# Optimization experiments

Measured on AMD Instinct MI355X. Metric: run time of the kernel, lower is better.

Reference implementation:

```python
import jax, jax.numpy as jnp
import numpy as np

B, G, NPA, NT, L = 8192, 689, 16, 131, 6
S = G + NPA * NT  # 2785 = 689 genes + 16 nodes per each of 131 assemblies


def setup_inputs() -> dict:
    key = jax.random.key(0)
    ks = jax.random.split(key, 8)
    x = jax.random.normal(ks[0], (B, G), dtype=jnp.float32)
    # depth-0 mask: place the 689 gene inputs into the first 689 slots of the layer
    lm0 = jnp.zeros((G, S), jnp.float32).at[jnp.arange(G), jnp.arange(G)].set(1.0)
    # per-depth sparse binary connectivity masks (ontology DAG edges at each depth)
    lm = (jax.random.uniform(ks[1], (L, S, S)) < 0.02).astype(jnp.float32)
    # diagonal pass-through masks for edges skipping this depth (stored as diagonals)
    flm_diag = (jax.random.uniform(ks[2], (L, S)) < 0.3).astype(jnp.float32)
    # final assembly selector: the nodes_per_assembly slots of the root assembly
    fasm = jnp.zeros((S,), jnp.float32).at[G:G + NPA].set(1.0)
    W0 = jax.random.normal(ks[3], (G, S), dtype=jnp.float32) * 0.05
    b0 = jnp.zeros((S,), jnp.float32)
    W = jax.random.normal(ks[4], (L, S, S), dtype=jnp.float32) * 0.05
    b = jnp.zeros((L, S), jnp.float32)
    gamma = jnp.ones((L + 1, S), jnp.float32)
    beta = jnp.zeros((L + 1, S), jnp.float32)
    w_out = jax.random.normal(ks[5], (S,), dtype=jnp.float32) * 0.05
    b_out = jnp.zeros((), jnp.float32)
    return {"x": x, "lm0": lm0, "lm": lm, "flm_diag": flm_diag, "fasm": fasm,
            "W0": W0, "b0": b0, "W": W, "b": b, "gamma": gamma, "beta": beta,
            "w_out": w_out, "b_out": b_out}


def _bn(h, g, bt, eps=1e-5):
    # training-mode BatchNorm1d over the batch axis
    m = h.mean(axis=0)
    v = h.var(axis=0)
    return (h - m) * jax.lax.rsqrt(v + eps) * g + bt


def reference(x, lm0, lm, flm_diag, fasm, W0, b0, W, b, gamma, beta, w_out, b_out):
    # depth 0: masked linear placing genes into layer slots, BN before activation
    h = jnp.tanh(_bn(x @ (W0 * lm0) + b0, gamma[0], beta[0]))  # [B, S]
    def step(h, layer):
        Wl, bl, lml, dl, gl, btl = layer
        # masked linear + BN + activation, plus diagonal pass-through skip
        hn = jnp.tanh(_bn(h @ (Wl * lml) + bl, gl, btl)) + h * dl
        return hn, None
    h, _ = jax.lax.scan(step, h, (W, b, lm, flm_diag, gamma[1:], beta[1:]))
    # output_method='final': linear head on final-assembly nodes only
    return (h * fasm) @ w_out + b_out  # [B]
```

## Files before the change

### kernel.cpp

```cpp
#include <hip/hip_runtime.h>
#include <hip/hip_fp16.h>
#include <stdint.h>

typedef uint32_t u32;
typedef uint64_t u64;
typedef unsigned int v4u __attribute__((ext_vector_type(4)));
typedef float v4f __attribute__((ext_vector_type(4)));
typedef _Float16 v2h __attribute__((ext_vector_type(2)));

constexpr int CB   = 8192;
constexpr int CG   = 689;
constexpr int CL   = 6;
constexpr int CS   = 2785;
constexpr int CSP  = 2816;
constexpr int CRS  = 8256;
constexpr int KCAP = 112;

union V16 { v4u u; v2h h2[4]; };
union F4  { v4f v; float f[4]; u32 u[4]; };
union HW  { u32 u; v2h h; };

__global__ __launch_bounds__(256) void build_main(const float* __restrict__ lm,
                                                  const float* __restrict__ W,
                                                  u64* __restrict__ ent,
                                                  int* __restrict__ cnt)
{
    int rb = blockIdx.x;
    int l  = rb / CS;
    int j  = rb - l * CS;
    const float* lrow = lm + (size_t)rb * CS;
    const float* wrow = W  + (size_t)rb * CS;
    u64 hi = ((u64)((u32)j * (u32)(CRS * 2))) << 32;
    int colbase = l * CSP;

    for (int s4 = threadIdx.x * 4; s4 < CS; s4 += 1024) {
        if (s4 + 4 <= CS) {
            F4 m4; m4.v = *reinterpret_cast<const v4f*>(lrow + s4);
            if ((m4.u[0] | m4.u[1] | m4.u[2] | m4.u[3]) == 0u) continue;
            F4 w4; w4.v = *reinterpret_cast<const v4f*>(wrow + s4);
#pragma unroll
            for (int q = 0; q < 4; q++) {
                if (m4.f[q] != 0.0f) {
                    int s = s4 + q;
                    int pos = atomicAdd(&cnt[colbase + s], 1);
                    if (pos < KCAP) {
                        u32 hw = (u32)__half_as_ushort(__float2half(w4.f[q]));
                        ent[(size_t)(colbase + s) * KCAP + pos] = hi | (u64)(hw | (hw << 16));
                    }
                }
            }
        } else {
            for (int s = s4; s < CS; s++) {
                float m = lrow[s];
                if (m != 0.0f) {
                    int pos = atomicAdd(&cnt[colbase + s], 1);
                    if (pos < KCAP) {
                        u32 hw = (u32)__half_as_ushort(__float2half(wrow[s]));
                        ent[(size_t)(colbase + s) * KCAP + pos] = hi | (u64)(hw | (hw << 16));
                    }
                }
            }
        }
    }
}

__global__ __launch_bounds__(256) void build0(const float* __restrict__ lm0,
                                              const float* __restrict__ W0,
                                              u64* __restrict__ ent,
                                              int* __restrict__ cnt)
{
    int j = blockIdx.x;
    const float* lrow = lm0 + (size_t)j * CS;
    const float* wrow = W0  + (size_t)j * CS;
    u64 hi = ((u64)((u32)j * (u32)(CRS * 2))) << 32;
    for (int s4 = threadIdx.x * 4; s4 < CS; s4 += 1024) {
        if (s4 + 4 <= CS) {
            F4 m4; m4.v = *reinterpret_cast<const v4f*>(lrow + s4);
            if ((m4.u[0] | m4.u[1] | m4.u[2] | m4.u[3]) == 0u) continue;
            F4 w4; w4.v = *reinterpret_cast<const v4f*>(wrow + s4);
#pragma unroll
            for (int q = 0; q < 4; q++) {
                if (m4.f[q] != 0.0f) {
                    int s = s4 + q;
                    int pos = atomicAdd(&cnt[s], 1);
                    if (pos < KCAP) {
                        u32 hw = (u32)__half_as_ushort(__float2half(w4.f[q]));
                        ent[(size_t)s * KCAP + pos] = hi | (u64)(hw | (hw << 16));
                    }
                }
            }
        } else {
            for (int s = s4; s < CS; s++) {
                float m = lrow[s];
                if (m != 0.0f) {
                    int pos = atomicAdd(&cnt[s], 1);
                    if (pos < KCAP) {
                        u32 hw = (u32)__half_as_ushort(__float2half(wrow[s]));
                        ent[(size_t)s * KCAP + pos] = hi | (u64)(hw | (hw << 16));
                    }
                }
            }
        }
    }
}

__global__ __launch_bounds__(256) void transpose_x(const float* __restrict__ x,
                                                   __half* __restrict__ xT)
{
    __shared__ float tile[32][33];
    int gx = blockIdx.x * 32;
    int gy = blockIdx.y * 32;
    int tx = threadIdx.x, ty = threadIdx.y;
#pragma unroll
    for (int i = 0; i < 32; i += 8) {
        int g = gx + tx;
        int b = gy + ty + i;
        tile[ty + i][tx] = (g < CG) ? x[(size_t)b * CG + g] : 0.f;
    }
    __syncthreads();
#pragma unroll
    for (int i = 0; i < 32; i += 8) {
        int g = gx + ty + i;
        int b = gy + tx;
        if (g < CG) xT[(size_t)g * CRS + b] = __float2half(tile[tx][ty + i]);
    }
}

__global__ __launch_bounds__(64) void gather_k(const __half* __restrict__ src,
                                               __half* __restrict__ dst,
                                               const u64* __restrict__ ent,
                                               const int* __restrict__ cnt,
                                               const float* __restrict__ bias,
                                               float* __restrict__ sumv,
                                               float* __restrict__ sumq,
                                               const int* __restrict__ sel,
                                               const int* __restrict__ selcnt)
{
    int s;
    if (sel) {
        if ((int)blockIdx.y >= *selcnt) return;
        s = sel[blockIdx.y];
    } else {
        s = blockIdx.y;
    }
    int lane = threadIdx.x;
    int boff = blockIdx.z * 4096 + blockIdx.x * 512 + lane * 8;

    int n = cnt[s]; if (n > KCAP) n = KCAP;
    int ng = (n + 7) >> 3;
    const u64* e = ent + (size_t)s * KCAP;
    const char* sb = (const char*)src + (size_t)boff * 2;

    float bv = bias[s];
    float acc[8];
#pragma unroll
    for (int j = 0; j < 8; j++) acc[j] = bv;

    for (int g = 0; g < ng; g++) {
        u64 ev[8];
#pragma unroll
        for (int q = 0; q < 8; q++) ev[q] = e[g * 8 + q];
        V16 rv[8];
#pragma unroll
        for (int q = 0; q < 8; q++)
            rv[q].u = *reinterpret_cast<const v4u*>(sb + (u32)(ev[q] >> 32));
#pragma unroll
        for (int q = 0; q < 8; q++) {
            HW w2; w2.u = (u32)ev[q];
#pragma unroll
            for (int j = 0; j < 4; j++) {
                float2 a2;
                a2.x = acc[2*j]; a2.y = acc[2*j+1];
#if __has_builtin(__builtin_amdgcn_fdot2)
#endif
                (void)a2;
                float2 f = __half22float2(*(const __half2*)&rv[q].h2[j]);
                float w = __half2float(*(const __half*)&w2.h);
                acc[2*j]   = fmaf(w, f.x, acc[2*j]);
                acc[2*j+1] = fmaf(w, f.y, acc[2*j+1]);
            }
        }
    }

    V16 o;
#pragma unroll
    for (int j = 0; j < 4; j++) {
        v2h p; p.x = (_Float16)acc[2*j]; p.y = (_Float16)acc[2*j+1];
        o.h2[j] = p;
    }
    __builtin_nontemporal_store(o.u, reinterpret_cast<v4u*>(dst + (size_t)s * CRS + boff));

    float ls = 0.f, lq = 0.f;
#pragma unroll
    for (int j = 0; j < 8; j++) { ls += acc[j]; lq += acc[j] * acc[j]; }
#pragma unroll
    for (int off = 32; off > 0; off >>= 1) {
        ls += __shfl_xor(ls, off);
        lq += __shfl_xor(lq, off);
    }
    if (lane == 0) { atomicAdd(&sumv[s], ls); atomicAdd(&sumq[s], lq); }
}

__global__ __launch_bounds__(64) void bn_act(__half* __restrict__ h,
                                             const __half* __restrict__ prev,
                                             const float* __restrict__ sumv,
                                             const float* __restrict__ sumq,
                                             const float* __restrict__ gamma,
                                             const float* __restrict__ beta,
                                             const float* __restrict__ dlv)
{
    int s = blockIdx.y;
    int boff = blockIdx.x * 512 + threadIdx.x * 8;
    float mean = sumv[s] * (1.0f / CB);
    float var  = sumq[s] * (1.0f / CB) - mean * mean;
    float rstd = rsqrtf(var + 1e-5f);
    float scale = gamma[s] * rstd;
    float shift = beta[s] - mean * scale;
    size_t base = (size_t)s * CRS + boff;
    V16 v; v.u = *reinterpret_cast<const v4u*>(h + base);
    V16 pv;
    float d = 0.f;
    if (prev) { d = dlv[s]; pv.u = *reinterpret_cast<const v4u*>(prev + base); }
    V16 o;
#pragma unroll
    for (int j = 0; j < 4; j++) {
        float2 f = __half22float2(*(const __half2*)&v.h2[j]);
        float t0 = tanhf(fmaf(f.x, scale, shift));
        float t1 = tanhf(fmaf(f.y, scale, shift));
        if (prev) {
            float2 p = __half22float2(*(const __half2*)&pv.h2[j]);
            t0 = fmaf(d, p.x, t0);
            t1 = fmaf(d, p.y, t1);
        }
        v2h pk; pk.x = (_Float16)t0; pk.y = (_Float16)t1;
        o.h2[j] = pk;
    }
    *reinterpret_cast<v4u*>(h + base) = o.u;
}

__global__ __launch_bounds__(256) void head_prep(const float* __restrict__ fasm,
                                                 const float* __restrict__ wout,
                                                 int* __restrict__ hcnt,
                                                 int* __restrict__ hs,
                                                 float* __restrict__ hc)
{
    int s = blockIdx.x * 256 + threadIdx.x;
    if (s >= CS) return;
    float c = fasm[s] * wout[s];
    if (c != 0.f) {
        int p = atomicAdd(hcnt, 1);
        if (p < 64) { hs[p] = s; hc[p] = c; }
    }
}

__global__ __launch_bounds__(256) void head_k(const __half* __restrict__ h6pre,
                                              const __half* __restrict__ h5,
                                              const int* __restrict__ hcnt,
                                              const int* __restrict__ hs,
                                              const float* __restrict__ hc,
                                              const float* __restrict__ sumv,
                                              const float* __restrict__ sumq,
                                              const float* __restrict__ gamma,
                                              const float* __restrict__ beta,
                                              const float* __restrict__ dlv,
                                              const float* __restrict__ bout,
                                              float* __restrict__ out)
{
    int b = blockIdx.x * 256 + threadIdx.x;
    int n = *hcnt; if (n > 64) n = 64;
    float acc = bout[0];
    for (int k = 0; k < n; k++) {
        int s = hs[k];
        float mean = sumv[s] * (1.0f / CB);
        float var  = sumq[s] * (1.0f / CB) - mean * mean;
        float rstd = rsqrtf(var + 1e-5f);
        float scale = gamma[s] * rstd;
        float shift = beta[s] - mean * scale;
        float pre  = __half2float(h6pre[(size_t)s * CRS + b]);
        float prev = __half2float(h5[(size_t)s * CRS + b]);
        float hn = tanhf(fmaf(pre, scale, shift)) + dlv[s] * prev;
        acc = fmaf(hc[k], hn, acc);
    }
    out[b] = acc;
}

extern "C" void kernel_launch(void* const* d_in, const int* in_sizes, int n_in,
                              void* d_out, int out_size, void* d_ws, size_t ws_size,
                              hipStream_t stream)
{
    const float* x    = (const float*)d_in[0];
    const float* lm0  = (const float*)d_in[1];
    const float* lm   = (const float*)d_in[2];
    const float* flm  = (const float*)d_in[3];
    const float* fasm = (const float*)d_in[4];
    const float* W0   = (const float*)d_in[5];
    const float* b0   = (const float*)d_in[6];
    const float* W    = (const float*)d_in[7];
    const float* bb   = (const float*)d_in[8];
    const float* gam  = (const float*)d_in[9];
    const float* bet  = (const float*)d_in[10];
    const float* wout = (const float*)d_in[11];
    const float* bout = (const float*)d_in[12];
    float* out = (float*)d_out;

    char* ws = (char*)d_ws;
    int*    cnt  = (int*)ws;
    float*  sumv = (float*)(ws + 78848);
    float*  sumq = (float*)(ws + 157696);
    int*    hcnt = (int*)(ws + 236544);
    int*    hs   = (int*)(ws + 236560);
    float*  hc   = (float*)(ws + 236816);
    u64*    ent  = (u64*)(ws + 237184);
    __half* hA   = (__half*)(ws + 17899136);
    __half* hB   = (__half*)(ws + 63885056);
    __half* xT   = hB;

    (void)hipMemsetAsync(ws, 0, 17899136, stream);

    build_main<<<dim3(CL * CS), 256, 0, stream>>>(lm, W, ent + (size_t)CSP * KCAP, cnt + CSP);
    build0    <<<dim3(CG),      256, 0, stream>>>(lm0, W0, ent, cnt);
    transpose_x<<<dim3(22, 256), dim3(32, 8), 0, stream>>>(x, xT);
    head_prep<<<dim3(11), 256, 0, stream>>>(fasm, wout, hcnt, hs, hc);

    const __half* cur = xT;
    __half* bufs[2] = {hA, hB};
    int which = 0;
    for (int t = 0; t < 6; t++) {
        __half* dst = bufs[which];
        const float* bias = (t == 0) ? b0 : bb + (size_t)(t - 1) * CS;
        gather_k<<<dim3(8, CS, 2), 64, 0, stream>>>(cur, dst,
            ent + (size_t)t * CSP * KCAP, cnt + t * CSP, bias,
            sumv + t * CSP, sumq + t * CSP, nullptr, nullptr);
        bn_act<<<dim3(16, CS), 64, 0, stream>>>(dst, (t == 0) ? nullptr : cur,
            sumv + t * CSP, sumq + t * CSP, gam + (size_t)t * CS, bet + (size_t)t * CS,
            (t == 0) ? nullptr : flm + (size_t)(t - 1) * CS);
        cur = dst;
        which ^= 1;
    }
    __half* h6 = bufs[which];
    gather_k<<<dim3(8, 16, 2), 64, 0, stream>>>(cur, h6,
        ent + (size_t)6 * CSP * KCAP, cnt + 6 * CSP, bb + (size_t)5 * CS,
        sumv + 6 * CSP, sumq + 6 * CSP, hs, hcnt);
    head_k<<<dim3(32), 256, 0, stream>>>(h6, cur, hcnt, hs, hc,
        sumv + 6 * CSP, sumq + 6 * CSP, gam + (size_t)6 * CS, bet + (size_t)6 * CS,
        flm + (size_t)5 * CS, bout, out);
}
```

Baseline: 1.199 ms.

## Build sparse column tables per tile in shared memory instead of global atomics

Replaces the two row-parallel table builders with one column-tiled kernel. Each block scans all rows for a 32-column tile, collects entries and counts with shared-memory atomics, then writes the whole tile out contiguously. This removes the global atomics and scattered 8-byte writes, and shrinks the large workspace memset to only the stats region. The cost is fewer blocks (88x7), each reading many rows with strided 16-byte accesses, which may reduce memory-level parallelism.

```diff
diff --git a/kernel.cpp b/kernel.cpp
--- a/kernel.cpp
+++ b/kernel.cpp
@@ -15,92 +15,88 @@
 constexpr int CSP  = 2816;
 constexpr int CRS  = 8256;
 constexpr int KCAP = 112;
+constexpr int TILE = 32;
+constexpr int NTIL = 88;
 
 union V16 { v4u u; v2h h2[4]; };
 union F4  { v4f v; float f[4]; u32 u[4]; };
 union HW  { u32 u; v2h h; };
 
-__global__ __launch_bounds__(256) void build_main(const float* __restrict__ lm,
-                                                  const float* __restrict__ W,
-                                                  u64* __restrict__ ent,
-                                                  int* __restrict__ cnt)
-{
-    int rb = blockIdx.x;
-    int l  = rb / CS;
-    int j  = rb - l * CS;
-    const float* lrow = lm + (size_t)rb * CS;
-    const float* wrow = W  + (size_t)rb * CS;
-    u64 hi = ((u64)((u32)j * (u32)(CRS * 2))) << 32;
-    int colbase = l * CSP;
-
-    for (int s4 = threadIdx.x * 4; s4 < CS; s4 += 1024) {
-        if (s4 + 4 <= CS) {
-            F4 m4; m4.v = *reinterpret_cast<const v4f*>(lrow + s4);
+__global__ __launch_bounds__(256) void build_tables(const float* __restrict__ lm0,
+                                                    const float* __restrict__ W0,
+                                                    const float* __restrict__ lm,
+                                                    const float* __restrict__ W,
+                                                    u64* __restrict__ ent,
+                                                    int* __restrict__ cnt)
+{
+    __shared__ u64 eL[TILE * KCAP];
+    __shared__ int cL[TILE];
+
+    int tbl  = blockIdx.y;
+    int x    = blockIdx.x;
+    int tile = (x & 7) * (NTIL / 8) + (x >> 3);
+    int s0   = tile * TILE;
+
+    const float* mbase; const float* wbase; int nrows;
+    if (tbl == 0) { mbase = lm0; wbase = W0; nrows = CG; }
+    else {
+        size_t off = (size_t)(tbl - 1) * CS * CS;
+        mbase = lm + off; wbase = W + off; nrows = CS;
+    }
+
+    int t = threadIdx.x;
+    for (int i = t; i < TILE * KCAP; i += 256) eL[i] = 0;
+    if (t < TILE) cL[t] = 0;
+    __syncthreads();
+
+    int rl = t >> 3;
+    int cq = (t & 7) * 4;
+    int c  = s0 + cq;
+    int np = (nrows + 31) >> 5;
+
+    for (int p = 0; p < np; p++) {
+        int r = p * 32 + rl;
+        if (r >= nrows) continue;
+        const float* mr = mbase + (size_t)r * CS;
+        if (c + 3 < CS) {
+            F4 m4; m4.v = *reinterpret_cast<const v4f*>(mr + c);
             if ((m4.u[0] | m4.u[1] | m4.u[2] | m4.u[3]) == 0u) continue;
-            F4 w4; w4.v = *reinterpret_cast<const v4f*>(wrow + s4);
+            F4 w4; w4.v = *reinterpret_cast<const v4f*>(wbase + (size_t)r * CS + c);
+            u64 hi = ((u64)((u32)r * (u32)(CRS * 2))) << 32;
 #pragma unroll
             for (int q = 0; q < 4; q++) {
                 if (m4.f[q] != 0.0f) {
-                    int s = s4 + q;
-                    int pos = atomicAdd(&cnt[colbase + s], 1);
+                    int pos = atomicAdd(&cL[cq + q], 1);
                     if (pos < KCAP) {
                         u32 hw = (u32)__half_as_ushort(__float2half(w4.f[q]));
-                        ent[(size_t)(colbase + s) * KCAP + pos] = hi | (u64)(hw | (hw << 16));
+                        eL[(cq + q) * KCAP + pos] = hi | (u64)(hw | (hw << 16));
                     }
                 }
             }
         } else {
-            for (int s = s4; s < CS; s++) {
-                float m = lrow[s];
+            u64 hi = ((u64)((u32)r * (u32)(CRS * 2))) << 32;
+            for (int q = 0; q < 4; q++) {
+                int cc = c + q;
+                if (cc >= CS) break;
+                float m = mr[cc];
                 if (m != 0.0f) {
-                    int pos = atomicAdd(&cnt[colbase + s], 1);
+                    int pos = atomicAdd(&cL[cq + q], 1);
                     if (pos < KCAP) {
-                        u32 hw = (u32)__half_as_ushort(__float2half(wrow[s]));
-                        ent[(size_t)(colbase + s) * KCAP + pos] = hi | (u64)(hw | (hw << 16));
+                        u32 hw = (u32)__half_as_ushort(__float2half(wbase[(size_t)r * CS + cc]));
+                        eL[(cq + q) * KCAP + pos] = hi | (u64)(hw | (hw << 16));
                     }
                 }
             }
         }
     }
-}
-
-__global__ __launch_bounds__(256) void build0(const float* __restrict__ lm0,
-                                              const float* __restrict__ W0,
-                                              u64* __restrict__ ent,
-                                              int* __restrict__ cnt)
-{
-    int j = blockIdx.x;
-    const float* lrow = lm0 + (size_t)j * CS;
-    const float* wrow = W0  + (size_t)j * CS;
-    u64 hi = ((u64)((u32)j * (u32)(CRS * 2))) << 32;
-    for (int s4 = threadIdx.x * 4; s4 < CS; s4 += 1024) {
-        if (s4 + 4 <= CS) {
-            F4 m4; m4.v = *reinterpret_cast<const v4f*>(lrow + s4);
-            if ((m4.u[0] | m4.u[1] | m4.u[2] | m4.u[3]) == 0u) continue;
-            F4 w4; w4.v = *reinterpret_cast<const v4f*>(wrow + s4);
-#pragma unroll
-            for (int q = 0; q < 4; q++) {
-                if (m4.f[q] != 0.0f) {
-                    int s = s4 + q;
-                    int pos = atomicAdd(&cnt[s], 1);
-                    if (pos < KCAP) {
-                        u32 hw = (u32)__half_as_ushort(__float2half(w4.f[q]));
-                        ent[(size_t)s * KCAP + pos] = hi | (u64)(hw | (hw << 16));
-                    }
-                }
-            }
-        } else {
-            for (int s = s4; s < CS; s++) {
-                float m = lrow[s];
-                if (m != 0.0f) {
-                    int pos = atomicAdd(&cnt[s], 1);
-                    if (pos < KCAP) {
-                        u32 hw = (u32)__half_as_ushort(__float2half(wrow[s]));
-                        ent[(size_t)s * KCAP + pos] = hi | (u64)(hw | (hw << 16));
-                    }
-                }
-            }
-        }
+    __syncthreads();
+
+    size_t gbase = (size_t)(tbl * CSP + s0) * KCAP;
+    for (int i = t; i < TILE * KCAP; i += 256)
+        ent[gbase + i] = eL[i];
+    if (t < TILE) {
+        int n = cL[t]; if (n > KCAP) n = KCAP;
+        cnt[tbl * CSP + s0 + t] = n;
     }
 }
 
@@ -169,11 +165,6 @@
             HW w2; w2.u = (u32)ev[q];
 #pragma unroll
             for (int j = 0; j < 4; j++) {
-                float2 a2;
-                a2.x = acc[2*j]; a2.y = acc[2*j+1];
-#if __has_builtin(__builtin_amdgcn_fdot2)
-#endif
-                (void)a2;
                 float2 f = __half22float2(*(const __half2*)&rv[q].h2[j]);
                 float w = __half2float(*(const __half*)&w2.h);
                 acc[2*j]   = fmaf(w, f.x, acc[2*j]);
@@ -315,10 +306,9 @@
     __half* hB   = (__half*)(ws + 63885056);
     __half* xT   = hB;
 
-    (void)hipMemsetAsync(ws, 0, 17899136, stream);
-
-    build_main<<<dim3(CL * CS), 256, 0, stream>>>(lm, W, ent + (size_t)CSP * KCAP, cnt + CSP);
-    build0    <<<dim3(CG),      256, 0, stream>>>(lm0, W0, ent, cnt);
+    (void)hipMemsetAsync(ws + 78848, 0, 158224, stream);
+
+    build_tables<<<dim3(NTIL, 7), 256, 0, stream>>>(lm0, W0, lm, W, ent, cnt);
     transpose_x<<<dim3(22, 256), dim3(32, 8), 0, stream>>>(x, xT);
     head_prep<<<dim3(11), 256, 0, stream>>>(fasm, wout, hcnt, hs, hc);
 
```

Result: no change. 1.193 ms (-0.6%).
